# Kernel optimization log

Measured on AMD Instinct MI355X. Metric: run time of the kernel, lower is better.

The kernel has to match this reference:

```python
import jax, jax.numpy as jnp
import numpy as np

N, B, E, H, G, L = 128, 2, 512, 1024, 50, 3
RBF_RADIUS = 12.0
AVG_LEN = 60.0


def _resmlp(h, Win, bin_, Wh, bh, Wout, bout):
    # input proj + activation, residual hidden blocks, linear head
    h = jax.nn.gelu(h @ Win + bin_, approximate=False)
    for i in range(Wh.shape[0]):  # fixed small number of layers
        h = h + jax.nn.gelu(h @ Wh[i] + bh[i], approximate=False)
    return h @ Wout + bout


def setup_inputs() -> dict:
    key = jax.random.key(0)
    ks = jax.random.split(key, 20)
    s_in = 1.0 / np.sqrt(3 * E)
    s_h = 1.0 / np.sqrt(H)
    s_g = 1.0 / np.sqrt(G)
    return {
        'x': jax.random.normal(ks[0], (N, B, E), jnp.float32),
        'dist': jax.random.uniform(ks[1], (N, N, B), jnp.float32),
        'vec_hat': jax.random.normal(ks[2], (N, N, B, 3), jnp.float32),
        'mask': jnp.ones((B, N), dtype=bool),
        'rbf_W': jax.random.normal(ks[3], (G, E), jnp.float32) * s_g,
        'rbf_b': jnp.zeros((E,), jnp.float32),
        'e_Win': jax.random.normal(ks[4], (3 * E, H), jnp.float32) * s_in,
        'e_bin': jnp.zeros((H,), jnp.float32),
        'e_Wh': jax.random.normal(ks[5], (L, H, H), jnp.float32) * s_h,
        'e_bh': jnp.zeros((L, H), jnp.float32),
        'e_Wout': jax.random.normal(ks[6], (H, 1), jnp.float32) * s_h,
        'e_bout': jnp.zeros((1,), jnp.float32),
        'f_Win': jax.random.normal(ks[7], (3 * E, H), jnp.float32) * s_in,
        'f_bin': jnp.zeros((H,), jnp.float32),
        'f_Wh': jax.random.normal(ks[8], (L, H, H), jnp.float32) * s_h,
        'f_bh': jnp.zeros((L, H), jnp.float32),
        'f_Wout': jax.random.normal(ks[9], (H, 1), jnp.float32) * s_h,
        'f_bout': jnp.zeros((1,), jnp.float32),
    }


def reference(x, dist, vec_hat, mask, rbf_W, rbf_b, e_Win, e_bin, e_Wh, e_bh,
              e_Wout, e_bout, f_Win, f_bin, f_Wh, f_bh, f_Wout, f_bout):
    # Gaussian RBF expansion + linear projection to embed_dim
    offset = jnp.linspace(0.0, RBF_RADIUS, G)
    coeff = -0.5 / (offset[1] - offset[0]) ** 2
    g = jnp.exp(coeff * (dist[..., None] - offset) ** 2)       # (N,N,B,G)
    rbf = g @ rbf_W + rbf_b                                    # (N,N,B,E)

    # all-pairs concat feature: [x_i, x_j, rbf_ij]  -> (N,N,B,3E)
    feat = jnp.concatenate([
        jnp.broadcast_to(x[:, None], rbf.shape),
        jnp.broadcast_to(x[None, :], rbf.shape),
        rbf,
    ], axis=-1)

    entries = (mask.T[:, None] & mask.T[None, :])[..., None].astype(feat.dtype)  # (N,N,B,1)

    energy_pairs = _resmlp(feat, e_Win, e_bin, e_Wh, e_bh, e_Wout, e_bout)       # (N,N,B,1)
    force_pairs = _resmlp(feat, f_Win, f_bin, f_Wh, f_bh, f_Wout, f_bout) * vec_hat  # (N,N,B,3)

    energy = (energy_pairs * entries).sum((0, 1)) / AVG_LEN ** 2  # (B,1)
    forces = (force_pairs * entries).sum(0) / AVG_LEN             # (N,B,3)
    # torch: forces.transpose(0,1)[mask]; mask is all-True here, so this is a reshape
    forces = jnp.swapaxes(forces, 0, 1).reshape(-1, 3)            # (B*N,3)
    return energy, forces
```

## Files before the change

kernel.cpp:

```cpp
#include <hip/hip_runtime.h>
#include <stdint.h>

typedef __bf16 bf16x8 __attribute__((ext_vector_type(8)));
typedef __bf16 bf16x4 __attribute__((ext_vector_type(4)));
typedef float  f32x4  __attribute__((ext_vector_type(4)));
typedef unsigned int u32;

__device__ __forceinline__ void gl_lds16(const void* gptr, void* lptr) {
    __builtin_amdgcn_global_load_lds(
        (const __attribute__((address_space(1))) u32*)gptr,
        (__attribute__((address_space(3))) u32*)lptr,
        16, 0, 0);
}

__device__ __forceinline__ float gelu_f(float x) {
    float u = 0.7978845608f * x * (1.0f + 0.044715f * x * x);
    float e = __expf(2.0f * u);
    float t = 1.0f - 2.0f / (e + 1.0f);
    return 0.5f * x * (1.0f + t);
}

#define MEMFENCE __asm__ __volatile__("" ::: "memory")

__global__ void zero_out(float* __restrict__ o, int n) {
    int i = blockIdx.x * 256 + threadIdx.x;
    if (i < n) o[i] = 0.0f;
}

__global__ __launch_bounds__(256)
void transpose_multi(const float* __restrict__ src0, const float* __restrict__ src1,
                     __bf16* __restrict__ dst0, __bf16* __restrict__ dst1,
                     int K, int Ncols, int perBranch) {
    const int z = blockIdx.z;
    const int branch = z / perBranch;
    const int l = z - branch * perBranch;
    const size_t elems = (size_t)K * Ncols;
    const float* src = (branch ? src1 : src0) + (size_t)l * elems;
    __bf16* dst = (branch ? dst1 : dst0) + (size_t)l * elems;

    __shared__ float tile[64][65];
    const int bk = blockIdx.x * 64;
    const int bn = blockIdx.y * 64;
    const int tid = threadIdx.x;
    const int tr = tid >> 4;
    const int tc = (tid & 15) * 4;
#pragma unroll
    for (int p = 0; p < 4; ++p) {
        const int r = tr + p * 16;
        float4 v = *(const float4*)&src[(size_t)(bk + r) * Ncols + bn + tc];
        tile[r][tc] = v.x; tile[r][tc + 1] = v.y;
        tile[r][tc + 2] = v.z; tile[r][tc + 3] = v.w;
    }
    __syncthreads();
#pragma unroll
    for (int p = 0; p < 4; ++p) {
        const int rn = tr + p * 16;
        bf16x4 o;
        o[0] = (__bf16)tile[tc + 0][rn];
        o[1] = (__bf16)tile[tc + 1][rn];
        o[2] = (__bf16)tile[tc + 2][rn];
        o[3] = (__bf16)tile[tc + 3][rn];
        *(bf16x4*)&dst[(size_t)(bn + rn) * K + bk + tc] = o;
    }
}

__global__ void f32_to_bf16(const float* __restrict__ s, __bf16* __restrict__ d, int n) {
    int idx = blockIdx.x * 256 + threadIdx.x;
    if (idx * 4 < n) {
        float4 v = *(const float4*)(s + idx * 4);
        bf16x4 o;
        o[0] = (__bf16)v.x; o[1] = (__bf16)v.y; o[2] = (__bf16)v.z; o[3] = (__bf16)v.w;
        *(bf16x4*)(d + idx * 4) = o;
    }
}

__global__ void build_M1(const float* __restrict__ rbfW, const float* __restrict__ rbf_b,
                         __bf16* __restrict__ M1) {
    int t = blockIdx.x * 256 + threadIdx.x;
    int r = t >> 8;
    int c = (t & 255) * 2;
    float v0 = 0.f, v1 = 0.f;
    if (r < 50)       { v0 = rbfW[r * 512 + c]; v1 = rbfW[r * 512 + c + 1]; }
    else if (r == 50) { v0 = rbf_b[c];          v1 = rbf_b[c + 1]; }
    M1[r * 512 + c] = (__bf16)v0;
    M1[r * 512 + c + 1] = (__bf16)v1;
}

__global__ __launch_bounds__(256)
void build_G(const float* __restrict__ dist, __bf16* __restrict__ G) {
    const int t = threadIdx.x;
    const int row = blockIdx.x * 32 + (t >> 3);
    const int c0 = (t & 7) * 8;
    const float sp = 12.0f / 49.0f;
    const float coeff = -0.5f / (sp * sp);
    const float d = dist[row];
    bf16x8 v;
#pragma unroll
    for (int q = 0; q < 8; ++q) {
        const int k = c0 + q;
        float val;
        if (k < 50)       { float tt = d - (float)k * sp; val = __expf(coeff * tt * tt); }
        else if (k == 50) val = 1.0f;
        else              val = 0.0f;
        v[q] = (__bf16)val;
    }
    *(bf16x8*)(G + (size_t)row * 64 + c0) = v;
}

template <int NK, int NBN, int MODE, bool DUAL, int MINW, bool SWZ>
__global__ __launch_bounds__(256, MINW)
void gemm_k(const __bf16* __restrict__ A0, const __bf16* __restrict__ A1,
            const __bf16* __restrict__ B0, const __bf16* __restrict__ B1,
            int lda, int ldb, int ldc,
            const float* __restrict__ bias0, const float* __restrict__ bias1,
            __bf16* __restrict__ C0, __bf16* __restrict__ C1,
            float* __restrict__ Cf0, float* __restrict__ Cf1,
            const float* __restrict__ P0, const float* __restrict__ P1,
            const float* __restrict__ wout0, const float* __restrict__ wout1,
            float* __restrict__ dot0, float* __restrict__ dot1) {
    constexpr int NBS = (NBN == 16) ? 4 : (NBN == 8) ? 3 : 0;
    __shared__ __align__(16) __bf16 As[3][128 * 32];
    __shared__ __align__(16) __bf16 Bs[3][128 * 32];

    const int tid = threadIdx.x;
    int bn, bm, branch = 0;
    if constexpr (SWZ) {
        const int x = blockIdx.x & 7;
        const int slot = blockIdx.x >> 3;
        bn = slot & (NBN - 1);
        int grp = x + ((slot >> NBS) << 3);
        if constexpr (DUAL) {
            const int half = (gridDim.x >> NBS) >> 1;
            branch = (grp >= half);
            if (branch) grp -= half;
        }
        bm = grp;
    } else {
        int f2 = blockIdx.x;
        if constexpr (DUAL) {
            const int half = gridDim.x >> 1;
            branch = (f2 >= half);
            if (branch) f2 -= half;
        }
        bn = f2 & (NBN - 1);
        bm = f2 >> NBS;
    }
    const int w = tid >> 6;
    const int lane = tid & 63;

    const __bf16* Ab = (DUAL && branch) ? A1 : A0;
    const __bf16* Bb = (DUAL && branch) ? B1 : B0;

    const int r0 = tid >> 2;
    const int s0 = tid & 3;
    const char* gA0 = (const char*)Ab + (size_t)(bm * 128 + r0) * lda + s0 * 16;
    const char* gA1 = gA0 + (size_t)64 * lda;
    const char* gB0 = (const char*)Bb + (size_t)(bn * 128 + r0) * ldb + s0 * 16;
    const char* gB1 = gB0 + (size_t)64 * ldb;

    char* lA0 = (char*)&As[0][0] + w * 1024;
    char* lA1 = (char*)&As[1][0] + w * 1024;
    char* lA2 = (char*)&As[2][0] + w * 1024;
    char* lB0 = (char*)&Bs[0][0] + w * 1024;
    char* lB1 = (char*)&Bs[1][0] + w * 1024;
    char* lB2 = (char*)&Bs[2][0] + w * 1024;

    const int wm = (w >> 1) & 1;
    const int wn = w & 1;
    const int lm = lane & 15;
    const int ko = (lane >> 4) << 3;
    const int fo = (wm * 64 + lm) * 32 + ko;
    const int go = (wn * 64 + lm) * 32 + ko;
    const __bf16* pA0 = &As[0][0] + fo;
    const __bf16* pA1 = &As[1][0] + fo;
    const __bf16* pA2 = &As[2][0] + fo;
    const __bf16* pB0 = &Bs[0][0] + go;
    const __bf16* pB1 = &Bs[1][0] + go;
    const __bf16* pB2 = &Bs[2][0] + go;

    f32x4 acc[4][4];
    const f32x4 zero = {0.0f, 0.0f, 0.0f, 0.0f};
#pragma unroll
    for (int i = 0; i < 4; ++i)
#pragma unroll
        for (int j = 0; j < 4; ++j) acc[i][j] = zero;

    auto stage = [&](int buf) {
        char* la = (buf == 0) ? lA0 : (buf == 1) ? lA1 : lA2;
        char* lb = (buf == 0) ? lB0 : (buf == 1) ? lB1 : lB2;
        gl_lds16(gA0, la); gl_lds16(gA1, la + 4096);
        gl_lds16(gB0, lb); gl_lds16(gB1, lb + 4096);
        gA0 += 64; gA1 += 64; gB0 += 64; gB1 += 64;
    };
    auto compute = [&](int buf) {
        const __bf16* pa = (buf == 0) ? pA0 : (buf == 1) ? pA1 : pA2;
        const __bf16* pb = (buf == 0) ? pB0 : (buf == 1) ? pB1 : pB2;
        bf16x8 af[4], bfg[4];
#pragma unroll
        for (int i = 0; i < 4; ++i) {
            af[i]  = *(const bf16x8*)(pa + i * 512);
            bfg[i] = *(const bf16x8*)(pb + i * 512);
        }
#pragma unroll
        for (int mi = 0; mi < 4; ++mi)
#pragma unroll
            for (int ni = 0; ni < 4; ++ni)
                acc[mi][ni] = __builtin_amdgcn_mfma_f32_16x16x32_bf16(
                    af[mi], bfg[ni], acc[mi][ni], 0, 0, 0);
    };
    auto iterstep = [&](int cbuf, int sbuf) {
        MEMFENCE;
        __builtin_amdgcn_s_waitcnt(0xF74);
        __builtin_amdgcn_s_barrier();
        MEMFENCE;
        compute(cbuf);
        MEMFENCE;
        stage(sbuf);
        MEMFENCE;
    };

    stage(0);
    stage(1);
    constexpr int NIT = NK - 2;
    constexpr int NG = NIT / 3;
    constexpr int NR = NIT % 3;
    for (int g = 0; g < NG; ++g) {
        iterstep(0, 2);
        iterstep(1, 0);
        iterstep(2, 1);
    }
    if constexpr (NR >= 1) iterstep(0, 2);
    if constexpr (NR >= 2) iterstep(1, 0);
    MEMFENCE;
    __builtin_amdgcn_s_waitcnt(0xF74);
    __builtin_amdgcn_s_barrier();
    MEMFENCE;
    compute((NK - 2) % 3);
    MEMFENCE;
    __builtin_amdgcn_s_waitcnt(0xF70);
    __builtin_amdgcn_s_barrier();
    MEMFENCE;
    compute((NK - 1) % 3);

    const int col0 = bn * 128 + wn * 64 + lm;
    const int row0 = bm * 128 + wm * 64 + ((lane >> 4) << 2);
    const int ldaE = lda >> 1;

    float rowdot[16];
    if constexpr (MODE == 1) {
#pragma unroll
        for (int q = 0; q < 16; ++q) rowdot[q] = 0.0f;
    }

    const bool side = (MODE == 2) && (bn >= 8);
    const float* bp = (MODE == 2) ? (side ? bias1 : bias0)
                                  : ((DUAL && branch) ? bias1 : bias0);
    __bf16* Cout = (MODE == 2) ? (side ? C1 : C0)
                               : ((DUAL && branch) ? C1 : C0);
    const float* woutb = (MODE == 1) ? ((DUAL && branch) ? wout1 : wout0) : nullptr;

#pragma unroll
    for (int ni = 0; ni < 4; ++ni) {
        const int gn = col0 + ni * 16;
        const int gnl = (MODE == 2) ? (gn & 1023) : gn;
        float bv = 0.0f;
        if constexpr (MODE <= 2) bv = bp[gnl];
        float wv = 0.0f;
        if constexpr (MODE == 1) wv = woutb[gn];

        float res[16];
        if constexpr (MODE == 0 || MODE == 1) {
#pragma unroll
            for (int mi = 0; mi < 4; ++mi)
#pragma unroll
                for (int rr = 0; rr < 4; ++rr)
                    res[mi * 4 + rr] =
                        (float)Ab[(size_t)(row0 + mi * 16 + rr) * ldaE + gn];
        } else if constexpr (MODE == 2) {
#pragma unroll
            for (int mi = 0; mi < 4; ++mi)
#pragma unroll
                for (int rr = 0; rr < 4; ++rr) {
                    const int gm = row0 + mi * 16 + rr;
                    const int p0row = ((gm >> 8) << 1) | (gm & 1);
                    const int p1row = gm & 255;
                    res[mi * 4 + rr] = P0[(size_t)p0row * 2048 + gn]
                                     + P1[(size_t)p1row * 2048 + gn];
                }
        }
        MEMFENCE;

#pragma unroll
        for (int mi = 0; mi < 4; ++mi) {
#pragma unroll
            for (int rr = 0; rr < 4; ++rr) {
                const int gm = row0 + mi * 16 + rr;
                const float a = acc[mi][ni][rr];
                if constexpr (MODE == 0) {
                    float v = gelu_f(a + bv) + res[mi * 4 + rr];
                    Cout[(size_t)gm * ldc + gn] = (__bf16)v;
                } else if constexpr (MODE == 1) {
                    float v = gelu_f(a + bv) + res[mi * 4 + rr];
                    rowdot[mi * 4 + rr] += v * wv;
                } else if constexpr (MODE == 2) {
                    float v = a + bv + res[mi * 4 + rr];
                    Cout[(size_t)gm * ldc + gnl] = (__bf16)gelu_f(v);
                } else if constexpr (MODE == 3) {
                    float* Cfw = (DUAL && branch) ? Cf1 : Cf0;
                    Cfw[(size_t)gm * ldc + gn] = a;
                } else {
                    C0[(size_t)gm * ldc + gn] = (__bf16)a;
                }
            }
        }
    }

    if constexpr (MODE == 1) {
#pragma unroll
        for (int s = 1; s < 16; s <<= 1)
#pragma unroll
            for (int q = 0; q < 16; ++q) rowdot[q] += __shfl_xor(rowdot[q], s);
        if (lm == 0) {
            float* dotb = (DUAL && branch) ? dot1 : dot0;
            float* dp = dotb + (size_t)(bn * 2 + wn) * 32768 + row0;
#pragma unroll
            for (int q = 0; q < 16; ++q)
                dp[(q >> 2) * 16 + (q & 3)] = rowdot[q];
        }
    }
}

#define WBAR(imm) do { MEMFENCE; __builtin_amdgcn_s_waitcnt(imm); \
                       __builtin_amdgcn_s_barrier(); MEMFENCE; } while (0)

template <int MODE, bool DUAL>
__global__ __launch_bounds__(512, 2)
void gemm256(const __bf16* __restrict__ A0, const __bf16* __restrict__ A1,
             const __bf16* __restrict__ B0, const __bf16* __restrict__ B1,
             const float* __restrict__ bias0, const float* __restrict__ bias1,
             __bf16* __restrict__ C0, __bf16* __restrict__ C1,
             const float* __restrict__ wout0, const float* __restrict__ wout1,
             float* __restrict__ dot0, float* __restrict__ dot1) {
    __shared__ __align__(16) char ldsbuf[131072];

    const int tid = threadIdx.x;
    const int nxg = gridDim.x >> 3;
    const int id = (blockIdx.x & 7) * nxg + (blockIdx.x >> 3);
    const int bn = id & 3;
    int rest = id >> 2;
    int branch = 0;
    if constexpr (DUAL) { branch = rest >> 7; rest &= 127; }
    const int bm = rest;

    const __bf16* __restrict__ Ab = (DUAL && branch) ? A1 : A0;
    const __bf16* __restrict__ Bb = (DUAL && branch) ? B1 : B0;

    const int w = tid >> 6;
    const int lane = tid & 63;

    const int srow = tid >> 2;
    const int scol = ((tid & 3) << 4) ^ (((tid >> 3) & 3) << 4);
    const char* gA = (const char*)Ab + (size_t)(bm * 256 + srow) * 2048 + scol;
    const char* gB = (const char*)Bb + (size_t)(bn * 256 + srow) * 2048 + scol;

    auto stageT = [&](int kt, int buf) {
        const size_t ko = (size_t)kt * 64;
        char* d = ldsbuf + buf * 32768 + w * 1024;
        gl_lds16(gA + ko,          d);
        gl_lds16(gA + ko + 262144, d + 8192);
        gl_lds16(gB + ko,          d + 16384);
        gl_lds16(gB + ko + 262144, d + 24576);
    };

    const int wm = w >> 2, wn = w & 3;
    const int lm = lane & 15, lq = lane >> 4;
    const int swz = ((lm >> 1) & 3) << 4;
    const int rA = (wm * 128 + lm) * 64 + ((lq * 16) ^ swz);
    const int rB = 16384 + (wn * 64 + lm) * 64 + ((lq * 16) ^ swz);

    f32x4 acc[8][4];
    const f32x4 zero = {0.0f, 0.0f, 0.0f, 0.0f};
#pragma unroll
    for (int i = 0; i < 8; ++i)
#pragma unroll
        for (int j = 0; j < 4; ++j) acc[i][j] = zero;

    auto body = [&](int kt, int cbuf, int sbuf, bool dostage) {
        const char* Lb = ldsbuf + cbuf * 32768;
        if (dostage) stageT(kt + 3, sbuf);
        MEMFENCE;
        bf16x8 a[8], b[4];
#pragma unroll
        for (int ni = 0; ni < 4; ++ni)
            b[ni] = *(const bf16x8*)(Lb + rB + ni * 1024);
#pragma unroll
        for (int mi = 0; mi < 8; ++mi)
            a[mi] = *(const bf16x8*)(Lb + rA + mi * 1024);
        __builtin_amdgcn_s_setprio(1);
#pragma unroll
        for (int mi = 0; mi < 4; ++mi)
#pragma unroll
            for (int ni = 0; ni < 4; ++ni)
                acc[mi][ni] = __builtin_amdgcn_mfma_f32_16x16x32_bf16(
                    a[mi], b[ni], acc[mi][ni], 0, 0, 0);
        __builtin_amdgcn_s_setprio(0);
        __builtin_amdgcn_s_setprio(1);
#pragma unroll
        for (int mi = 4; mi < 8; ++mi)
#pragma unroll
            for (int ni = 0; ni < 4; ++ni)
                acc[mi][ni] = __builtin_amdgcn_mfma_f32_16x16x32_bf16(
                    a[mi], b[ni], acc[mi][ni], 0, 0, 0);
        __builtin_amdgcn_s_setprio(0);
    };

    stageT(0, 0);
    stageT(1, 1);
    stageT(2, 2);
    for (int g = 0; g < 7; ++g) {
        const int k0 = g * 4;
        WBAR(0xF78); body(k0 + 0, 0, 3, true);
        WBAR(0xF78); body(k0 + 1, 1, 0, true);
        WBAR(0xF78); body(k0 + 2, 2, 1, true);
        WBAR(0xF78); body(k0 + 3, 3, 2, true);
    }
    WBAR(0xF78); body(28, 0, 3, true);
    WBAR(0xF78); body(29, 1, 0, false);
    WBAR(0xF74); body(30, 2, 1, false);
    WBAR(0xF70); body(31, 3, 2, false);

    const int row0 = bm * 256 + wm * 128 + lq * 4;
    const int col0 = bn * 256 + wn * 64 + lm;
    const float* __restrict__ bp = (DUAL && branch) ? bias1 : bias0;
    float bv[4];
#pragma unroll
    for (int ni = 0; ni < 4; ++ni) bv[ni] = bp[col0 + ni * 16];

    if constexpr (MODE == 0) {
        __bf16* __restrict__ Cw = (DUAL && branch) ? C1 : C0;
#pragma unroll
        for (int mi = 0; mi < 8; ++mi) {
            float res[16];
#pragma unroll
            for (int ni = 0; ni < 4; ++ni)
#pragma unroll
                for (int rr = 0; rr < 4; ++rr)
                    res[ni * 4 + rr] =
                        (float)Ab[(size_t)(row0 + mi * 16 + rr) * 1024 + col0 + ni * 16];
            MEMFENCE;
#pragma unroll
            for (int ni = 0; ni < 4; ++ni)
#pragma unroll
                for (int rr = 0; rr < 4; ++rr) {
                    float v = gelu_f(acc[mi][ni][rr] + bv[ni]) + res[ni * 4 + rr];
                    Cw[(size_t)(row0 + mi * 16 + rr) * 1024 + col0 + ni * 16] = (__bf16)v;
                }
        }
    } else {
        const float* __restrict__ wb = (DUAL && branch) ? wout1 : wout0;
        float wv[4];
#pragma unroll
        for (int ni = 0; ni < 4; ++ni) wv[ni] = wb[col0 + ni * 16];
        float rowdot[32];
#pragma unroll
        for (int q = 0; q < 32; ++q) rowdot[q] = 0.0f;
#pragma unroll
        for (int mi = 0; mi < 8; ++mi) {
            float res[16];
#pragma unroll
            for (int ni = 0; ni < 4; ++ni)
#pragma unroll
                for (int rr = 0; rr < 4; ++rr)
                    res[ni * 4 + rr] =
                        (float)Ab[(size_t)(row0 + mi * 16 + rr) * 1024 + col0 + ni * 16];
            MEMFENCE;
#pragma unroll
            for (int ni = 0; ni < 4; ++ni)
#pragma unroll
                for (int rr = 0; rr < 4; ++rr) {
                    float v = gelu_f(acc[mi][ni][rr] + bv[ni]) + res[ni * 4 + rr];
                    rowdot[mi * 4 + rr] += v * wv[ni];
                }
        }
#pragma unroll
        for (int s = 1; s < 16; s <<= 1)
#pragma unroll
            for (int q = 0; q < 32; ++q) rowdot[q] += __shfl_xor(rowdot[q], s);
        if (lm == 0) {
            float* __restrict__ db = (DUAL && branch) ? dot1 : dot0;
            float* dp = db + (size_t)(bn * 4 + wn) * 32768 + bm * 256 + wm * 128;
#pragma unroll
            for (int mi = 0; mi < 8; ++mi)
#pragma unroll
                for (int rr = 0; rr < 4; ++rr)
                    dp[mi * 16 + lq * 4 + rr] = rowdot[mi * 4 + rr];
        }
    }
}

__global__ __launch_bounds__(128)
void finalize(const float* __restrict__ dot_e, const float* __restrict__ dot_f,
              const float* __restrict__ eb, const float* __restrict__ fb,
              const float* __restrict__ vec, float* __restrict__ out) {
    const int bj = blockIdx.x;
    const int bb = bj >> 7, jj = bj & 127;
    const int i = threadIdx.x;
    const int m = (i * 128 + jj) * 2 + bb;
    float e = eb[0], f = fb[0];
#pragma unroll
    for (int s = 0; s < 16; ++s) {
        e += dot_e[(size_t)s * 32768 + m];
        f += dot_f[(size_t)s * 32768 + m];
    }
    f *= (1.0f / 60.0f);
    float fx = f * vec[(size_t)m * 3 + 0];
    float fy = f * vec[(size_t)m * 3 + 1];
    float fz = f * vec[(size_t)m * 3 + 2];
#pragma unroll
    for (int off = 32; off > 0; off >>= 1) {
        e  += __shfl_down(e, off);
        fx += __shfl_down(fx, off);
        fy += __shfl_down(fy, off);
        fz += __shfl_down(fz, off);
    }
    __shared__ float red[2][4];
    const int wv = i >> 6, lane = i & 63;
    if (lane == 0) { red[wv][0] = e; red[wv][1] = fx; red[wv][2] = fy; red[wv][3] = fz; }
    __syncthreads();
    if (i == 0) {
        atomicAdd(&out[bb], (red[0][0] + red[1][0]) * (1.0f / 3600.0f));
        float* fo = out + 2 + bj * 3;
        fo[0] = red[0][1] + red[1][1];
        fo[1] = red[0][2] + red[1][2];
        fo[2] = red[0][3] + red[1][3];
    }
}

extern "C" void kernel_launch(void* const* d_in, const int* in_sizes, int n_in,
                              void* d_out, int out_size, void* d_ws, size_t ws_size,
                              hipStream_t stream) {
    const float* x     = (const float*)d_in[0];
    const float* dist  = (const float*)d_in[1];
    const float* vec   = (const float*)d_in[2];
    const float* rbfW  = (const float*)d_in[4];
    const float* rbf_b = (const float*)d_in[5];
    const float* eWin  = (const float*)d_in[6];
    const float* ebin  = (const float*)d_in[7];
    const float* eWh   = (const float*)d_in[8];
    const float* ebh   = (const float*)d_in[9];
    const float* eWout = (const float*)d_in[10];
    const float* ebout = (const float*)d_in[11];
    const float* fWin  = (const float*)d_in[12];
    const float* fbin  = (const float*)d_in[13];
    const float* fWh   = (const float*)d_in[14];
    const float* fbh   = (const float*)d_in[15];
    const float* fWout = (const float*)d_in[16];
    const float* fbout = (const float*)d_in[17];
    float* out = (float*)d_out;

    char* p = (char*)d_ws;
    __bf16* WinTcat = (__bf16*)p;
    __bf16* eWinT = WinTcat;          p += (size_t)1024 * 1536 * 2;
    __bf16* fWinT = (__bf16*)p;       p += (size_t)1024 * 1536 * 2;
    __bf16* eWhT0 = (__bf16*)p;       p += (size_t)3 * 1024 * 1024 * 2;
    __bf16* fWhT0 = (__bf16*)p;       p += (size_t)3 * 1024 * 1024 * 2;
    __bf16* xb  = (__bf16*)p;         p += (size_t)256 * 512 * 2;
    __bf16* M1  = (__bf16*)p;         p += (size_t)128 * 512 * 2;
    __bf16* WgT = (__bf16*)p;         p += (size_t)2048 * 128 * 2;
    __bf16* G   = (__bf16*)p;         p += (size_t)32768 * 64 * 2;
    float* P0   = (float*)p;          p += (size_t)256 * 2048 * 4;
    float* P1   = (float*)p;          p += (size_t)256 * 2048 * 4;
    float* dot_e = (float*)p;         p += (size_t)16 * 32768 * 4;
    float* dot_f = (float*)p;         p += (size_t)16 * 32768 * 4;
    const size_t SLAB = (size_t)32768 * 1024 * 2;
    __bf16* he0 = (__bf16*)p;         p += SLAB;
    __bf16* hf0 = (__bf16*)p;         p += SLAB;
    __bf16* hAe = (__bf16*)p;         p += SLAB;
    __bf16* hAf = hAe;
    const bool dualHidden = ((size_t)(p - (char*)d_ws) + SLAB) <= ws_size;
    if (dualHidden) hAf = (__bf16*)p;

    zero_out<<<dim3(4), dim3(256), 0, stream>>>(out, 770);

    transpose_multi<<<dim3(24, 16, 2), dim3(256), 0, stream>>>(
        eWin, fWin, eWinT, fWinT, 1536, 1024, 1);
    transpose_multi<<<dim3(16, 16, 6), dim3(256), 0, stream>>>(
        eWh, fWh, eWhT0, fWhT0, 1024, 1024, 3);
    f32_to_bf16<<<dim3(128), dim3(256), 0, stream>>>(x, xb, 131072);
    build_M1<<<dim3(128), dim3(256), 0, stream>>>(rbfW, rbf_b, M1);
    build_G<<<dim3(1024), dim3(256), 0, stream>>>(dist, G);

    const dim3 blk(256);
    gemm_k<16, 16, 3, true, 3, false><<<dim3(64), blk, 0, stream>>>(
        xb, xb, WinTcat, WinTcat + 512, 1024, 3072, 2048,
        nullptr, nullptr, nullptr, nullptr, P0, P1,
        nullptr, nullptr, nullptr, nullptr, nullptr, nullptr);
    gemm_k<16, 1, 4, false, 3, false><<<dim3(16), blk, 0, stream>>>(
        WinTcat + 1024, nullptr, M1, nullptr, 3072, 1024, 128,
        nullptr, nullptr, WgT, nullptr, nullptr, nullptr,
        nullptr, nullptr, nullptr, nullptr, nullptr, nullptr);
    gemm_k<2, 16, 2, false, 3, true><<<dim3(4096), blk, 0, stream>>>(
        G, nullptr, WgT, nullptr, 128, 256, 1024,
        ebin, fbin, he0, hf0, nullptr, nullptr, P0, P1,
        nullptr, nullptr, nullptr, nullptr);

    const dim3 blk512(512);
    if (dualHidden) {
        gemm256<0, true><<<dim3(1024), blk512, 0, stream>>>(
            he0, hf0, eWhT0, fWhT0, ebh + 0, fbh + 0,
            hAe, hAf, nullptr, nullptr, nullptr, nullptr);
        gemm256<0, true><<<dim3(1024), blk512, 0, stream>>>(
            hAe, hAf, eWhT0 + (size_t)1048576, fWhT0 + (size_t)1048576,
            ebh + 1024, fbh + 1024, he0, hf0, nullptr, nullptr, nullptr, nullptr);
        gemm256<1, true><<<dim3(1024), blk512, 0, stream>>>(
            he0, hf0, eWhT0 + (size_t)2 * 1048576, fWhT0 + (size_t)2 * 1048576,
            ebh + 2048, fbh + 2048, nullptr, nullptr,
            eWout, fWout, dot_e, dot_f);
    } else {
        gemm256<0, false><<<dim3(512), blk512, 0, stream>>>(
            he0, nullptr, eWhT0, nullptr, ebh + 0, nullptr,
            hAe, nullptr, nullptr, nullptr, nullptr, nullptr);
        gemm256<0, false><<<dim3(512), blk512, 0, stream>>>(
            hAe, nullptr, eWhT0 + (size_t)1048576, nullptr, ebh + 1024, nullptr,
            he0, nullptr, nullptr, nullptr, nullptr, nullptr);
        gemm256<1, false><<<dim3(512), blk512, 0, stream>>>(
            he0, nullptr, eWhT0 + (size_t)2 * 1048576, nullptr, ebh + 2048, nullptr,
            nullptr, nullptr, eWout, nullptr, dot_e, nullptr);
        gemm256<0, false><<<dim3(512), blk512, 0, stream>>>(
            hf0, nullptr, fWhT0, nullptr, fbh + 0, nullptr,
            hAf, nullptr, nullptr, nullptr, nullptr, nullptr);
        gemm256<0, false><<<dim3(512), blk512, 0, stream>>>(
            hAf, nullptr, fWhT0 + (size_t)1048576, nullptr, fbh + 1024, nullptr,
            hf0, nullptr, nullptr, nullptr, nullptr, nullptr);
        gemm256<1, false><<<dim3(512), blk512, 0, stream>>>(
            hf0, nullptr, fWhT0 + (size_t)2 * 1048576, nullptr, fbh + 2048, nullptr,
            nullptr, nullptr, fWout, nullptr, dot_f, nullptr);
    }

    finalize<<<dim3(256), dim3(128), 0, stream>>>(dot_e, dot_f, ebout, fbout, vec, out);
}
```

Measured before the change: 748.4 us.

## Make hidden-layer GEMM persistent with cross-tile prefetch and transposed MFMA epilogue

The hidden-layer GEMM now runs as a persistent kernel with 256 blocks, each handling NITER output tiles in sequence. The first K-slices of the next tile are prefetched into LDS while the last slices of the current tile are still computing, which hides pipeline fill and drain between tiles. MFMA operands are swapped so each lane holds four consecutive columns, allowing vectorized bias, residual and output loads/stores and a cheaper row-dot reduction. The cost is higher register pressure from keeping tile state live, and fewer blocks in flight.

```diff
diff --git a/kernel.cpp b/kernel.cpp
--- a/kernel.cpp
+++ b/kernel.cpp
@@ -333,7 +333,7 @@
 #define WBAR(imm) do { MEMFENCE; __builtin_amdgcn_s_waitcnt(imm); \
                        __builtin_amdgcn_s_barrier(); MEMFENCE; } while (0)
 
-template <int MODE, bool DUAL>
+template <int MODE, bool DUAL, int NITER>
 __global__ __launch_bounds__(512, 2)
 void gemm256(const __bf16* __restrict__ A0, const __bf16* __restrict__ A1,
              const __bf16* __restrict__ B0, const __bf16* __restrict__ B1,
@@ -344,50 +344,55 @@
     __shared__ __align__(16) char ldsbuf[131072];
 
     const int tid = threadIdx.x;
-    const int nxg = gridDim.x >> 3;
-    const int id = (blockIdx.x & 7) * nxg + (blockIdx.x >> 3);
-    const int bn = id & 3;
-    int rest = id >> 2;
-    int branch = 0;
-    if constexpr (DUAL) { branch = rest >> 7; rest &= 127; }
-    const int bm = rest;
-
-    const __bf16* __restrict__ Ab = (DUAL && branch) ? A1 : A0;
-    const __bf16* __restrict__ Bb = (DUAL && branch) ? B1 : B0;
-
     const int w = tid >> 6;
     const int lane = tid & 63;
+    const int wm = w >> 2, wn = w & 3;
+    const int lm = lane & 15, lq = lane >> 4;
 
     const int srow = tid >> 2;
     const int scol = ((tid & 3) << 4) ^ (((tid >> 3) & 3) << 4);
+
+    const __bf16 *Ab, *Bb;
+    int bm, bn, branch;
+    auto decode = [&](int t) {
+        constexpr int VG = 256 * NITER;
+        const int v = t * 256 + blockIdx.x;
+        const int id = (v & 7) * (VG >> 3) + (v >> 3);
+        bn = id & 3;
+        int rest = id >> 2;
+        branch = 0;
+        if constexpr (DUAL) { branch = rest >> 7; rest &= 127; }
+        bm = rest;
+        Ab = (DUAL && branch) ? A1 : A0;
+        Bb = (DUAL && branch) ? B1 : B0;
+    };
+
+    decode(0);
     const char* gA = (const char*)Ab + (size_t)(bm * 256 + srow) * 2048 + scol;
     const char* gB = (const char*)Bb + (size_t)(bn * 256 + srow) * 2048 + scol;
 
-    auto stageT = [&](int kt, int buf) {
+    auto stageT = [&](const char* a, const char* b, int kt, int buf) {
         const size_t ko = (size_t)kt * 64;
         char* d = ldsbuf + buf * 32768 + w * 1024;
-        gl_lds16(gA + ko,          d);
-        gl_lds16(gA + ko + 262144, d + 8192);
-        gl_lds16(gB + ko,          d + 16384);
-        gl_lds16(gB + ko + 262144, d + 24576);
+        gl_lds16(a + ko,          d);
+        gl_lds16(a + ko + 262144, d + 8192);
+        gl_lds16(b + ko,          d + 16384);
+        gl_lds16(b + ko + 262144, d + 24576);
     };
 
-    const int wm = w >> 2, wn = w & 3;
-    const int lm = lane & 15, lq = lane >> 4;
     const int swz = ((lm >> 1) & 3) << 4;
     const int rA = (wm * 128 + lm) * 64 + ((lq * 16) ^ swz);
     const int rB = 16384 + (wn * 64 + lm) * 64 + ((lq * 16) ^ swz);
 
-    f32x4 acc[8][4];
+    f32x4 acc[4][8];
     const f32x4 zero = {0.0f, 0.0f, 0.0f, 0.0f};
 #pragma unroll
-    for (int i = 0; i < 8; ++i)
-#pragma unroll
-        for (int j = 0; j < 4; ++j) acc[i][j] = zero;
-
-    auto body = [&](int kt, int cbuf, int sbuf, bool dostage) {
+    for (int i = 0; i < 4; ++i)
+#pragma unroll
+        for (int j = 0; j < 8; ++j) acc[i][j] = zero;
+
+    auto body = [&](int cbuf) {
         const char* Lb = ldsbuf + cbuf * 32768;
-        if (dostage) stageT(kt + 3, sbuf);
         MEMFENCE;
         bf16x8 a[8], b[4];
 #pragma unroll
@@ -398,102 +403,119 @@
             a[mi] = *(const bf16x8*)(Lb + rA + mi * 1024);
         __builtin_amdgcn_s_setprio(1);
 #pragma unroll
-        for (int mi = 0; mi < 4; ++mi)
-#pragma unroll
-            for (int ni = 0; ni < 4; ++ni)
-                acc[mi][ni] = __builtin_amdgcn_mfma_f32_16x16x32_bf16(
-                    a[mi], b[ni], acc[mi][ni], 0, 0, 0);
-        __builtin_amdgcn_s_setprio(0);
-        __builtin_amdgcn_s_setprio(1);
-#pragma unroll
-        for (int mi = 4; mi < 8; ++mi)
-#pragma unroll
-            for (int ni = 0; ni < 4; ++ni)
-                acc[mi][ni] = __builtin_amdgcn_mfma_f32_16x16x32_bf16(
-                    a[mi], b[ni], acc[mi][ni], 0, 0, 0);
+        for (int ni = 0; ni < 4; ++ni)
+#pragma unroll
+            for (int mi = 0; mi < 8; ++mi)
+                acc[ni][mi] = __builtin_amdgcn_mfma_f32_16x16x32_bf16(
+                    b[ni], a[mi], acc[ni][mi], 0, 0, 0);
         __builtin_amdgcn_s_setprio(0);
     };
 
-    stageT(0, 0);
-    stageT(1, 1);
-    stageT(2, 2);
-    for (int g = 0; g < 7; ++g) {
-        const int k0 = g * 4;
-        WBAR(0xF78); body(k0 + 0, 0, 3, true);
-        WBAR(0xF78); body(k0 + 1, 1, 0, true);
-        WBAR(0xF78); body(k0 + 2, 2, 1, true);
-        WBAR(0xF78); body(k0 + 3, 3, 2, true);
-    }
-    WBAR(0xF78); body(28, 0, 3, true);
-    WBAR(0xF78); body(29, 1, 0, false);
-    WBAR(0xF74); body(30, 2, 1, false);
-    WBAR(0xF70); body(31, 3, 2, false);
-
-    const int row0 = bm * 256 + wm * 128 + lq * 4;
-    const int col0 = bn * 256 + wn * 64 + lm;
-    const float* __restrict__ bp = (DUAL && branch) ? bias1 : bias0;
-    float bv[4];
-#pragma unroll
-    for (int ni = 0; ni < 4; ++ni) bv[ni] = bp[col0 + ni * 16];
-
-    if constexpr (MODE == 0) {
-        __bf16* __restrict__ Cw = (DUAL && branch) ? C1 : C0;
-#pragma unroll
-        for (int mi = 0; mi < 8; ++mi) {
-            float res[16];
+    stageT(gA, gB, 0, 0);
+    stageT(gA, gB, 1, 1);
+    stageT(gA, gB, 2, 2);
+
+    for (int t = 0; t < NITER; ++t) {
+        const bool lastt = (t == NITER - 1);
+        for (int g = 0; g < 7; ++g) {
+            const int k0 = g * 4;
+            WBAR(0xF78); stageT(gA, gB, k0 + 3, 3); body(0);
+            WBAR(0xF78); stageT(gA, gB, k0 + 4, 0); body(1);
+            WBAR(0xF78); stageT(gA, gB, k0 + 5, 1); body(2);
+            WBAR(0xF78); stageT(gA, gB, k0 + 6, 2); body(3);
+        }
+        WBAR(0xF78); stageT(gA, gB, 31, 3); body(0);
+
+        const __bf16* Ab_e = Ab;
+        const int bm_e = bm, bn_e = bn, br_e = branch;
+        if (!lastt) {
+            decode(t + 1);
+            gA = (const char*)Ab + (size_t)(bm * 256 + srow) * 2048 + scol;
+            gB = (const char*)Bb + (size_t)(bn * 256 + srow) * 2048 + scol;
+            WBAR(0xF78); stageT(gA, gB, 0, 0); body(1);
+            WBAR(0xF78); stageT(gA, gB, 1, 1); body(2);
+            WBAR(0xF78); stageT(gA, gB, 2, 2); body(3);
+        } else {
+            WBAR(0xF78); body(1);
+            WBAR(0xF74); body(2);
+            WBAR(0xF70); body(3);
+        }
+
+        const int nbase = bn_e * 256 + wn * 64 + lq * 4;
+        const float* __restrict__ bp = (DUAL && br_e) ? bias1 : bias0;
+        f32x4 bv[4];
+#pragma unroll
+        for (int ni = 0; ni < 4; ++ni)
+            bv[ni] = *(const f32x4*)&bp[nbase + ni * 16];
+
+        if constexpr (MODE == 0) {
+            __bf16* __restrict__ Cw = (DUAL && br_e) ? C1 : C0;
+#pragma unroll
+            for (int mi = 0; mi < 8; ++mi) {
+                const size_t rb =
+                    (size_t)(bm_e * 256 + wm * 128 + mi * 16 + lm) * 1024;
+                bf16x4 res[4];
+#pragma unroll
+                for (int ni = 0; ni < 4; ++ni)
+                    res[ni] = *(const bf16x4*)&Ab_e[rb + nbase + ni * 16];
+                MEMFENCE;
+#pragma unroll
+                for (int ni = 0; ni < 4; ++ni) {
+                    bf16x4 o;
+#pragma unroll
+                    for (int r = 0; r < 4; ++r)
+                        o[r] = (__bf16)(gelu_f(acc[ni][mi][r] + bv[ni][r]) +
+                                        (float)res[ni][r]);
+                    *(bf16x4*)&Cw[rb + nbase + ni * 16] = o;
+                }
+            }
+        } else {
+            const float* __restrict__ wb = (DUAL && br_e) ? wout1 : wout0;
+            f32x4 wv[4];
 #pragma unroll
             for (int ni = 0; ni < 4; ++ni)
-#pragma unroll
-                for (int rr = 0; rr < 4; ++rr)
-                    res[ni * 4 + rr] =
-                        (float)Ab[(size_t)(row0 + mi * 16 + rr) * 1024 + col0 + ni * 16];
-            MEMFENCE;
-#pragma unroll
-            for (int ni = 0; ni < 4; ++ni)
-#pragma unroll
-                for (int rr = 0; rr < 4; ++rr) {
-                    float v = gelu_f(acc[mi][ni][rr] + bv[ni]) + res[ni * 4 + rr];
-                    Cw[(size_t)(row0 + mi * 16 + rr) * 1024 + col0 + ni * 16] = (__bf16)v;
-                }
-        }
-    } else {
-        const float* __restrict__ wb = (DUAL && branch) ? wout1 : wout0;
-        float wv[4];
-#pragma unroll
-        for (int ni = 0; ni < 4; ++ni) wv[ni] = wb[col0 + ni * 16];
-        float rowdot[32];
-#pragma unroll
-        for (int q = 0; q < 32; ++q) rowdot[q] = 0.0f;
-#pragma unroll
-        for (int mi = 0; mi < 8; ++mi) {
-            float res[16];
-#pragma unroll
-            for (int ni = 0; ni < 4; ++ni)
-#pragma unroll
-                for (int rr = 0; rr < 4; ++rr)
-                    res[ni * 4 + rr] =
-                        (float)Ab[(size_t)(row0 + mi * 16 + rr) * 1024 + col0 + ni * 16];
-            MEMFENCE;
-#pragma unroll
-            for (int ni = 0; ni < 4; ++ni)
-#pragma unroll
-                for (int rr = 0; rr < 4; ++rr) {
-                    float v = gelu_f(acc[mi][ni][rr] + bv[ni]) + res[ni * 4 + rr];
-                    rowdot[mi * 4 + rr] += v * wv[ni];
-                }
-        }
-#pragma unroll
-        for (int s = 1; s < 16; s <<= 1)
-#pragma unroll
-            for (int q = 0; q < 32; ++q) rowdot[q] += __shfl_xor(rowdot[q], s);
-        if (lm == 0) {
-            float* __restrict__ db = (DUAL && branch) ? dot1 : dot0;
-            float* dp = db + (size_t)(bn * 4 + wn) * 32768 + bm * 256 + wm * 128;
-#pragma unroll
-            for (int mi = 0; mi < 8; ++mi)
-#pragma unroll
-                for (int rr = 0; rr < 4; ++rr)
-                    dp[mi * 16 + lq * 4 + rr] = rowdot[mi * 4 + rr];
+                wv[ni] = *(const f32x4*)&wb[nbase + ni * 16];
+            float rd[8];
+#pragma unroll
+            for (int q = 0; q < 8; ++q) rd[q] = 0.0f;
+#pragma unroll
+            for (int mi = 0; mi < 8; ++mi) {
+                const size_t rb =
+                    (size_t)(bm_e * 256 + wm * 128 + mi * 16 + lm) * 1024;
+                bf16x4 res[4];
+#pragma unroll
+                for (int ni = 0; ni < 4; ++ni)
+                    res[ni] = *(const bf16x4*)&Ab_e[rb + nbase + ni * 16];
+                MEMFENCE;
+#pragma unroll
+                for (int ni = 0; ni < 4; ++ni)
+#pragma unroll
+                    for (int r = 0; r < 4; ++r) {
+                        float v = gelu_f(acc[ni][mi][r] + bv[ni][r]) +
+                                  (float)res[ni][r];
+                        rd[mi] += v * wv[ni][r];
+                    }
+            }
+#pragma unroll
+            for (int mi = 0; mi < 8; ++mi) {
+                rd[mi] += __shfl_xor(rd[mi], 16);
+                rd[mi] += __shfl_xor(rd[mi], 32);
+            }
+            if (lq == 0) {
+                float* __restrict__ db = (DUAL && br_e) ? dot1 : dot0;
+                float* dp = db + (size_t)(bn_e * 4 + wn) * 32768 +
+                            bm_e * 256 + wm * 128;
+#pragma unroll
+                for (int mi = 0; mi < 8; ++mi)
+                    dp[mi * 16 + lm] = rd[mi];
+            }
+        }
+
+        if (!lastt) {
+#pragma unroll
+            for (int i = 0; i < 4; ++i)
+#pragma unroll
+                for (int j = 0; j < 8; ++j) acc[i][j] = zero;
         }
     }
 }
@@ -605,34 +627,35 @@
         nullptr, nullptr, nullptr, nullptr);
 
     const dim3 blk512(512);
+    const dim3 grid256(256);
     if (dualHidden) {
-        gemm256<0, true><<<dim3(1024), blk512, 0, stream>>>(
+        gemm256<0, true, 4><<<grid256, blk512, 0, stream>>>(
             he0, hf0, eWhT0, fWhT0, ebh + 0, fbh + 0,
             hAe, hAf, nullptr, nullptr, nullptr, nullptr);
-        gemm256<0, true><<<dim3(1024), blk512, 0, stream>>>(
+        gemm256<0, true, 4><<<grid256, blk512, 0, stream>>>(
             hAe, hAf, eWhT0 + (size_t)1048576, fWhT0 + (size_t)1048576,
             ebh + 1024, fbh + 1024, he0, hf0, nullptr, nullptr, nullptr, nullptr);
-        gemm256<1, true><<<dim3(1024), blk512, 0, stream>>>(
+        gemm256<1, true, 4><<<grid256, blk512, 0, stream>>>(
             he0, hf0, eWhT0 + (size_t)2 * 1048576, fWhT0 + (size_t)2 * 1048576,
             ebh + 2048, fbh + 2048, nullptr, nullptr,
             eWout, fWout, dot_e, dot_f);
     } else {
-        gemm256<0, false><<<dim3(512), blk512, 0, stream>>>(
+        gemm256<0, false, 2><<<grid256, blk512, 0, stream>>>(
             he0, nullptr, eWhT0, nullptr, ebh + 0, nullptr,
             hAe, nullptr, nullptr, nullptr, nullptr, nullptr);
-        gemm256<0, false><<<dim3(512), blk512, 0, stream>>>(
+        gemm256<0, false, 2><<<grid256, blk512, 0, stream>>>(
             hAe, nullptr, eWhT0 + (size_t)1048576, nullptr, ebh + 1024, nullptr,
             he0, nullptr, nullptr, nullptr, nullptr, nullptr);
-        gemm256<1, false><<<dim3(512), blk512, 0, stream>>>(
+        gemm256<1, false, 2><<<grid256, blk512, 0, stream>>>(
             he0, nullptr, eWhT0 + (size_t)2 * 1048576, nullptr, ebh + 2048, nullptr,
             nullptr, nullptr, eWout, nullptr, dot_e, nullptr);
-        gemm256<0, false><<<dim3(512), blk512, 0, stream>>>(
+        gemm256<0, false, 2><<<grid256, blk512, 0, stream>>>(
             hf0, nullptr, fWhT0, nullptr, fbh + 0, nullptr,
             hAf, nullptr, nullptr, nullptr, nullptr, nullptr);
-        gemm256<0, false><<<dim3(512), blk512, 0, stream>>>(
+        gemm256<0, false, 2><<<grid256, blk512, 0, stream>>>(
             hAf, nullptr, fWhT0 + (size_t)1048576, nullptr, fbh + 1024, nullptr,
             hf0, nullptr, nullptr, nullptr, nullptr, nullptr);
-        gemm256<1, false><<<dim3(512), blk512, 0, stream>>>(
+        gemm256<1, false, 2><<<grid256, blk512, 0, stream>>>(
             hf0, nullptr, fWhT0 + (size_t)2 * 1048576, nullptr, fbh + 2048, nullptr,
             nullptr, nullptr, fWout, nullptr, dot_f, nullptr);
     }
```

Measured after the change: 1.037 ms. 1.39x slower.
